# Performance work log

Hardware: AMD Instinct MI355X
Metric: run time of the kernel (lower is better)

The kernel has to match this reference:

```python
import jax, jax.numpy as jnp
import numpy as np

N_NODES = 50000
N_EDGES = 800000
IN_DIM = 128
HID = 256
HEADS = 4
OUT_DIM = 128
NEG_SLOPE = 0.2


def gat_conv(x, src, dst, W, a_src, a_dst, b, heads, out_ch):
    """PyG-style GATConv: per-edge attention + segment softmax over dst."""
    N = x.shape[0]
    h = (x @ W).reshape(N, heads, out_ch)              # [N,H,C]
    alph_s = jnp.einsum('nhc,hc->nh', h, a_src)        # [N,H]
    alph_d = jnp.einsum('nhc,hc->nh', h, a_dst)        # [N,H]
    e = jax.nn.leaky_relu(alph_s[src] + alph_d[dst], NEG_SLOPE)  # [E,H]
    m = jax.lax.stop_gradient(jax.ops.segment_max(e, dst, num_segments=N))
    ex = jnp.exp(e - m[dst])
    s = jax.ops.segment_sum(ex, dst, num_segments=N)
    alpha = ex / (s[dst] + 1e-16)                      # [E,H]
    out = jax.ops.segment_sum(h[src] * alpha[:, :, None], dst, num_segments=N)
    return out.reshape(N, heads * out_ch) + b


def setup_inputs() -> dict:
    key = jax.random.key(0)
    ks = jax.random.split(key, 12)
    x = jax.random.normal(ks[0], (N_NODES, IN_DIM), dtype=jnp.float32)
    edge_index = jax.random.randint(ks[1], (2, N_EDGES), 0, N_NODES, dtype=jnp.int64)
    c1 = HID // HEADS  # 64
    sc1 = 1.0 / np.sqrt(IN_DIM)
    sc2 = 1.0 / np.sqrt(HID)
    W1 = jax.random.normal(ks[2], (IN_DIM, HID), dtype=jnp.float32) * sc1
    a1_src = jax.random.normal(ks[3], (HEADS, c1), dtype=jnp.float32) * sc1
    a1_dst = jax.random.normal(ks[4], (HEADS, c1), dtype=jnp.float32) * sc1
    b1 = jnp.zeros((HID,), dtype=jnp.float32)
    W2 = jax.random.normal(ks[5], (HID, OUT_DIM), dtype=jnp.float32) * sc2
    a2_src = jax.random.normal(ks[6], (1, OUT_DIM), dtype=jnp.float32) * sc2
    a2_dst = jax.random.normal(ks[7], (1, OUT_DIM), dtype=jnp.float32) * sc2
    b2 = jnp.zeros((OUT_DIM,), dtype=jnp.float32)
    return {"x": x, "edge_index": edge_index, "W1": W1, "a1_src": a1_src,
            "a1_dst": a1_dst, "b1": b1, "W2": W2, "a2_src": a2_src,
            "a2_dst": a2_dst, "b2": b2}


def reference(x, edge_index, W1, a1_src, a1_dst, b1, W2, a2_src, a2_dst, b2):
    N = x.shape[0]
    loops = jnp.arange(N, dtype=edge_index.dtype)
    # PyG default add_self_loops=True
    src = jnp.concatenate([edge_index[0], loops])
    dst = jnp.concatenate([edge_index[1], loops])
    h = jax.nn.relu(gat_conv(x, src, dst, W1, a1_src, a1_dst, b1, HEADS, HID // HEADS))
    # dropout is identity in eval mode
    return gat_conv(h, src, dst, W2, a2_src, a2_dst, b2, 1, OUT_DIM)
```

## Files before the change

kernel.cpp:

```cpp
#include <hip/hip_runtime.h>
#include <math.h>

#define NEG_SLOPE 0.2f
#define SLOTS 64

typedef __attribute__((ext_vector_type(8))) short bf16x8;
typedef __attribute__((ext_vector_type(4))) float f32x4;
typedef __attribute__((ext_vector_type(2))) float f32x2;

__device__ __forceinline__ float lrelu(float t) {
    return t > 0.f ? t : NEG_SLOPE * t;
}
__device__ __forceinline__ unsigned short f2bf(float f) {
    unsigned u = __float_as_uint(f);
    unsigned r = (u + 0x7fff + ((u >> 16) & 1)) >> 16;
    return (unsigned short)r;
}
__device__ __forceinline__ f32x2 unpack2(unsigned v) {
    f32x2 r;
    r.x = __uint_as_float(v << 16);
    r.y = __uint_as_float(v & 0xffff0000u);
    return r;
}

__global__ void prep(const float* __restrict__ x, unsigned* __restrict__ x_bf2,
                     const float* __restrict__ W1, unsigned short* __restrict__ W1t,
                     const float* __restrict__ W2, unsigned short* __restrict__ W2t,
                     const float* __restrict__ a1s, const float* __restrict__ a1d,
                     float* __restrict__ vsd1,
                     const float* __restrict__ a2s, const float* __restrict__ a2d,
                     float* __restrict__ vsd2,
                     int* __restrict__ cursor, int* __restrict__ eSrc,
                     long nx2, int N, int n0, int n1, int n2, int n3, int n4) {
    const int b = blockIdx.x, t = threadIdx.x;
    if (b < n0) {
        long i = (long)b * 256 + t;
        if (i < nx2) {
            float2 v = ((const float2*)x)[i];
            x_bf2[i] = (unsigned)f2bf(v.x) | ((unsigned)f2bf(v.y) << 16);
        }
    } else if (b < n1) {
        int i = (b - n0) * 256 + t;
        if (i < 256 * 128) {
            int n = i / 128, k = i % 128;
            W1t[i] = f2bf(W1[k * 256 + n]);
        }
    } else if (b < n2) {
        int i = (b - n1) * 256 + t;
        if (i < 128 * 256) {
            int n = i / 256, k = i % 256;
            W2t[i] = f2bf(W2[k * 128 + n]);
        }
    } else if (b < n3) {
        int i = (b - n2) * 256 + t;
        if (i < 512) {
            int k = i / 4, h = i % 4;
            float s = 0.f, d = 0.f;
            for (int c = 0; c < 64; c++) {
                float wv = W1[k * 256 + h * 64 + c];
                s += wv * a1s[h * 64 + c];
                d += wv * a1d[h * 64 + c];
            }
            vsd1[h * 128 + k] = s;
            vsd1[(4 + h) * 128 + k] = d;
        }
    } else if (b < n4) {
        int i = (b - n3) * 256 + t;
        if (i < 256) {
            float s = 0.f, d = 0.f;
            for (int c = 0; c < 128; c++) {
                float wv = W2[i * 128 + c];
                s += wv * a2s[c];
                d += wv * a2d[c];
            }
            vsd2[i] = s;
            vsd2[256 + i] = d;
        }
    } else {
        int i = (b - n4) * 256 + t;
        if (i < N) {
            cursor[i] = 1;
            eSrc[i << 6] = i;
        }
    }
}

__global__ void scatter_edges(const int* __restrict__ src, const int* __restrict__ dst,
                              int* __restrict__ cursor, int* __restrict__ eSrc, int E) {
    int e = blockIdx.x * blockDim.x + threadIdx.x;
    if (e < E) {
        int d = dst[e];
        int pos = atomicAdd(&cursor[d], 1);
        if (pos < SLOTS) eSrc[(d << 6) + pos] = src[e];
    }
}

template <int K, int H>
__global__ void gemv_attn(const float* __restrict__ X, const float* __restrict__ vsd,
                          float* __restrict__ as_, float* __restrict__ ad_, int M) {
    __shared__ float vs[2 * H * K];
    int t = threadIdx.x;
    for (int i = t; i < 2 * H * K; i += 256) vs[i] = vsd[i];
    __syncthreads();
    int wave = t >> 6, lane = t & 63;
    int n = blockIdx.x * 4 + wave;
    if (n >= M) return;
    float acc[2 * H];
#pragma unroll
    for (int j = 0; j < 2 * H; j++) acc[j] = 0.f;
#pragma unroll
    for (int i = 0; i < K / 64; i++) {
        float xv = X[(size_t)n * K + i * 64 + lane];
#pragma unroll
        for (int j = 0; j < 2 * H; j++) acc[j] += xv * vs[j * K + i * 64 + lane];
    }
#pragma unroll
    for (int off = 32; off > 0; off >>= 1) {
#pragma unroll
        for (int j = 0; j < 2 * H; j++) acc[j] += __shfl_down(acc[j], off, 64);
    }
    if (lane == 0) {
#pragma unroll
        for (int h = 0; h < H; h++) {
            as_[n * H + h] = acc[h];
            ad_[n * H + h] = acc[H + h];
        }
    }
}

template <int K, int N>
__global__ __launch_bounds__(256) void gemm_mfma(const unsigned short* __restrict__ A,
                                                 const unsigned short* __restrict__ Bt,
                                                 unsigned short* __restrict__ Cb, int M) {
    constexpr int LDT = 72;
    __shared__ __align__(16) short As[128 * LDT];
    __shared__ __align__(16) short Bs[64 * LDT];
    const int t = threadIdx.x;
    const int wave = t >> 6, lane = t & 63;
    const int row0 = blockIdx.x * 128;
    const int n0 = blockIdx.y * 64;

    f32x4 acc[2][4];
#pragma unroll
    for (int mt = 0; mt < 2; mt++)
#pragma unroll
        for (int nt = 0; nt < 4; nt++) acc[mt][nt] = (f32x4){0.f, 0.f, 0.f, 0.f};

    const int r = t >> 3, c8 = (t & 7) * 8;
    for (int kc = 0; kc < K; kc += 64) {
        const unsigned short* srcA = A + (size_t)row0 * K + kc;
#pragma unroll
        for (int p = 0; p < 4; p++) {
            int rr = r + p * 32;
            *(bf16x8*)&As[rr * LDT + c8] = *(const bf16x8*)&srcA[(size_t)rr * K + c8];
        }
        const unsigned short* srcB = Bt + (size_t)n0 * K + kc;
#pragma unroll
        for (int p = 0; p < 2; p++) {
            int rr = r + p * 32;
            *(bf16x8*)&Bs[rr * LDT + c8] = *(const bf16x8*)&srcB[(size_t)rr * K + c8];
        }
        __syncthreads();

        const int mbase = wave * 32 + (lane & 15);
        const int quad = lane >> 4;
#pragma unroll
        for (int ks = 0; ks < 2; ks++) {
            int ko = ks * 32 + quad * 8;
            bf16x8 a0 = *(const bf16x8*)&As[mbase * LDT + ko];
            bf16x8 a1 = *(const bf16x8*)&As[(mbase + 16) * LDT + ko];
#pragma unroll
            for (int nt = 0; nt < 4; nt++) {
                bf16x8 b = *(const bf16x8*)&Bs[((lane & 15) + nt * 16) * LDT + ko];
                acc[0][nt] = __builtin_amdgcn_mfma_f32_16x16x32_bf16(a0, b, acc[0][nt], 0, 0, 0);
                acc[1][nt] = __builtin_amdgcn_mfma_f32_16x16x32_bf16(a1, b, acc[1][nt], 0, 0, 0);
            }
        }
        __syncthreads();
    }

    const int colb = n0 + (lane & 15);
    const int rquad = (lane >> 4) * 4;
#pragma unroll
    for (int mt = 0; mt < 2; mt++) {
        int rb = row0 + wave * 32 + mt * 16 + rquad;
#pragma unroll
        for (int nt = 0; nt < 4; nt++) {
#pragma unroll
            for (int rr2 = 0; rr2 < 4; rr2++) {
                int row = rb + rr2;
                if (row < M) Cb[(size_t)row * N + colb + nt * 16] = f2bf(acc[mt][nt][rr2]);
            }
        }
    }
}

__global__ __launch_bounds__(256) void gemm1_head(
    const unsigned short* __restrict__ agg, const unsigned short* __restrict__ W1t,
    const float* __restrict__ b1, const float* __restrict__ vsd2,
    unsigned short* __restrict__ out1b, float* __restrict__ as2, float* __restrict__ ad2,
    int M, int Mpad) {
    constexpr int K = 128, LDT = 72;
    __shared__ __align__(16) short As[128 * LDT];
    __shared__ __align__(16) short Bs[64 * LDT];
    const int t = threadIdx.x;
    const int wave = t >> 6, lane = t & 63;
    const int row0 = blockIdx.x * 128;
    const int h = blockIdx.y;
    const unsigned short* A = agg + (size_t)h * Mpad * K;
    const unsigned short* Bt = W1t + (size_t)h * 64 * K;

    f32x4 acc[2][4];
#pragma unroll
    for (int mt = 0; mt < 2; mt++)
#pragma unroll
        for (int nt = 0; nt < 4; nt++) acc[mt][nt] = (f32x4){0.f, 0.f, 0.f, 0.f};

    const int r = t >> 3, c8 = (t & 7) * 8;
    for (int kc = 0; kc < K; kc += 64) {
        const unsigned short* srcA = A + (size_t)row0 * K + kc;
#pragma unroll
        for (int p = 0; p < 4; p++) {
            int rr = r + p * 32;
            *(bf16x8*)&As[rr * LDT + c8] = *(const bf16x8*)&srcA[(size_t)rr * K + c8];
        }
        const unsigned short* srcB = Bt + kc;
#pragma unroll
        for (int p = 0; p < 2; p++) {
            int rr = r + p * 32;
            *(bf16x8*)&Bs[rr * LDT + c8] = *(const bf16x8*)&srcB[(size_t)rr * K + c8];
        }
        __syncthreads();

        const int mbase = wave * 32 + (lane & 15);
        const int quad = lane >> 4;
#pragma unroll
        for (int ks = 0; ks < 2; ks++) {
            int ko = ks * 32 + quad * 8;
            bf16x8 a0 = *(const bf16x8*)&As[mbase * LDT + ko];
            bf16x8 a1 = *(const bf16x8*)&As[(mbase + 16) * LDT + ko];
#pragma unroll
            for (int nt = 0; nt < 4; nt++) {
                bf16x8 b = *(const bf16x8*)&Bs[((lane & 15) + nt * 16) * LDT + ko];
                acc[0][nt] = __builtin_amdgcn_mfma_f32_16x16x32_bf16(a0, b, acc[0][nt], 0, 0, 0);
                acc[1][nt] = __builtin_amdgcn_mfma_f32_16x16x32_bf16(a1, b, acc[1][nt], 0, 0, 0);
            }
        }
        __syncthreads();
    }

    const int col16 = lane & 15;
    const int grp = lane >> 4;
#pragma unroll
    for (int mt = 0; mt < 2; mt++) {
        int rb = row0 + wave * 32 + mt * 16 + grp * 4;
#pragma unroll
        for (int rr = 0; rr < 4; rr++) {
            int row = rb + rr;
            float ps = 0.f, pd = 0.f;
#pragma unroll
            for (int nt = 0; nt < 4; nt++) {
                int cg = h * 64 + col16 + nt * 16;
                float rres = acc[mt][nt][rr] + b1[cg];
                rres = fmaxf(rres, 0.f);
                if (row < M) out1b[(size_t)row * 256 + cg] = f2bf(rres);
                ps += rres * vsd2[cg];
                pd += rres * vsd2[256 + cg];
            }
#pragma unroll
            for (int mask = 1; mask < 16; mask <<= 1) {
                ps += __shfl_xor(ps, mask, 64);
                pd += __shfl_xor(pd, mask, 64);
            }
            if (col16 == 0 && row < M) {
                atomicAdd(&as2[row], ps);
                atomicAdd(&ad2[row], pd);
            }
        }
    }
}

__global__ __launch_bounds__(256) void fused_gather1(
    const int* __restrict__ cursor, const int* __restrict__ eSrc,
    const unsigned short* __restrict__ Xb,
    const float* __restrict__ as_, const float* __restrict__ ad_,
    unsigned short* __restrict__ agg, int N, int Mpad) {
    const int wv = threadIdx.x >> 6, lane = threadIdx.x & 63;
    const int half = lane >> 5, hl = lane & 31;
    const int d = blockIdx.x * 8 + wv * 2 + half;

    __shared__ float4 alS[4][2][64];
    __shared__ int offS[4][2][64];

    const bool vn = d < N;
    int deg = 0;
    if (vn) { deg = cursor[d]; if (deg > SLOTS) deg = SLOTS; }
    float4 adv = make_float4(0.f, 0.f, 0.f, 0.f);
    if (vn) adv = ((const float4*)ad_)[d];

    const int beg = d << 6;
    const int j0 = hl, j1 = hl + 32;
    const bool a0 = j0 < deg, a1 = j1 < deg;
    int s0 = vn ? d : 0, s1 = vn ? d : 0;
    if (a0) s0 = eSrc[beg + j0];
    if (a1) s1 = eSrc[beg + j1];
    float4 q0 = make_float4(0.f, 0.f, 0.f, 0.f), q1 = q0;
    if (a0) q0 = ((const float4*)as_)[s0];
    if (a1) q1 = ((const float4*)as_)[s1];

    float qa0[4] = {q0.x, q0.y, q0.z, q0.w};
    float qa1[4] = {q1.x, q1.y, q1.z, q1.w};
    float ad4[4] = {adv.x, adv.y, adv.z, adv.w};
    float e0[4], e1[4], m[4];
#pragma unroll
    for (int h = 0; h < 4; h++) {
        e0[h] = a0 ? lrelu(qa0[h] + ad4[h]) : -1e30f;
        e1[h] = a1 ? lrelu(qa1[h] + ad4[h]) : -1e30f;
        m[h] = fmaxf(e0[h], e1[h]);
    }
#pragma unroll
    for (int off = 1; off < 32; off <<= 1)
#pragma unroll
        for (int h = 0; h < 4; h++) m[h] = fmaxf(m[h], __shfl_xor(m[h], off, 64));
    float x0[4], x1[4], sum[4];
#pragma unroll
    for (int h = 0; h < 4; h++) {
        x0[h] = a0 ? __expf(e0[h] - m[h]) : 0.f;
        x1[h] = a1 ? __expf(e1[h] - m[h]) : 0.f;
        sum[h] = x0[h] + x1[h];
    }
#pragma unroll
    for (int off = 1; off < 32; off <<= 1)
#pragma unroll
        for (int h = 0; h < 4; h++) sum[h] += __shfl_xor(sum[h], off, 64);
    float ri[4];
#pragma unroll
    for (int h = 0; h < 4; h++) ri[h] = 1.f / (sum[h] + 1e-16f);

    alS[wv][half][j0] = make_float4(x0[0] * ri[0], x0[1] * ri[1], x0[2] * ri[2], x0[3] * ri[3]);
    alS[wv][half][j1] = make_float4(x1[0] * ri[0], x1[1] * ri[1], x1[2] * ri[2], x1[3] * ri[3]);
    offS[wv][half][j0] = s0 << 8;
    offS[wv][half][j1] = s1 << 8;

    int dmax = deg;
    { int o = __shfl_xor(dmax, 32, 64); dmax = dmax > o ? dmax : o; }

    const char* Xc = (const char*)Xb;
    const int myoff = hl * 8;
    f32x2 acc[4][2];
#pragma unroll
    for (int h = 0; h < 4; h++) { acc[h][0] = (f32x2){0.f, 0.f}; acc[h][1] = (f32x2){0.f, 0.f}; }

    int j = 0;
    for (; j + 3 < dmax; j += 4) {
        int o0 = offS[wv][half][j], o1 = offS[wv][half][j + 1];
        int o2 = offS[wv][half][j + 2], o3 = offS[wv][half][j + 3];
        uint2 v0 = *(const uint2*)(Xc + o0 + myoff);
        uint2 v1 = *(const uint2*)(Xc + o1 + myoff);
        uint2 v2 = *(const uint2*)(Xc + o2 + myoff);
        uint2 v3 = *(const uint2*)(Xc + o3 + myoff);
        float4 al0 = alS[wv][half][j];
        float4 al1 = alS[wv][half][j + 1];
        float4 al2 = alS[wv][half][j + 2];
        float4 al3 = alS[wv][half][j + 3];
        {
            f32x2 lo = unpack2(v0.x), hi = unpack2(v0.y);
            acc[0][0] += al0.x * lo; acc[0][1] += al0.x * hi;
            acc[1][0] += al0.y * lo; acc[1][1] += al0.y * hi;
            acc[2][0] += al0.z * lo; acc[2][1] += al0.z * hi;
            acc[3][0] += al0.w * lo; acc[3][1] += al0.w * hi;
        }
        {
            f32x2 lo = unpack2(v1.x), hi = unpack2(v1.y);
            acc[0][0] += al1.x * lo; acc[0][1] += al1.x * hi;
            acc[1][0] += al1.y * lo; acc[1][1] += al1.y * hi;
            acc[2][0] += al1.z * lo; acc[2][1] += al1.z * hi;
            acc[3][0] += al1.w * lo; acc[3][1] += al1.w * hi;
        }
        {
            f32x2 lo = unpack2(v2.x), hi = unpack2(v2.y);
            acc[0][0] += al2.x * lo; acc[0][1] += al2.x * hi;
            acc[1][0] += al2.y * lo; acc[1][1] += al2.y * hi;
            acc[2][0] += al2.z * lo; acc[2][1] += al2.z * hi;
            acc[3][0] += al2.w * lo; acc[3][1] += al2.w * hi;
        }
        {
            f32x2 lo = unpack2(v3.x), hi = unpack2(v3.y);
            acc[0][0] += al3.x * lo; acc[0][1] += al3.x * hi;
            acc[1][0] += al3.y * lo; acc[1][1] += al3.y * hi;
            acc[2][0] += al3.z * lo; acc[2][1] += al3.z * hi;
            acc[3][0] += al3.w * lo; acc[3][1] += al3.w * hi;
        }
    }
    for (; j < dmax; j++) {
        int o0 = offS[wv][half][j];
        uint2 v0 = *(const uint2*)(Xc + o0 + myoff);
        float4 al0 = alS[wv][half][j];
        f32x2 lo = unpack2(v0.x), hi = unpack2(v0.y);
        acc[0][0] += al0.x * lo; acc[0][1] += al0.x * hi;
        acc[1][0] += al0.y * lo; acc[1][1] += al0.y * hi;
        acc[2][0] += al0.z * lo; acc[2][1] += al0.z * hi;
        acc[3][0] += al0.w * lo; acc[3][1] += al0.w * hi;
    }

    if (vn) {
#pragma unroll
        for (int h = 0; h < 4; h++) {
            uint2 pack;
            pack.x = (unsigned)f2bf(acc[h][0].x) | ((unsigned)f2bf(acc[h][0].y) << 16);
            pack.y = (unsigned)f2bf(acc[h][1].x) | ((unsigned)f2bf(acc[h][1].y) << 16);
            ((uint2*)(agg + ((size_t)h * Mpad + d) * 128))[hl] = pack;
        }
    }
}

__global__ __launch_bounds__(256) void fused_gather2(
    const int* __restrict__ cursor, const int* __restrict__ eSrc,
    const unsigned short* __restrict__ Hb,
    const float* __restrict__ as_, const float* __restrict__ ad_,
    const float* __restrict__ b2, float* __restrict__ out, int N) {
    const int wv = threadIdx.x >> 6, lane = threadIdx.x & 63;
    const int half = lane >> 5, hl = lane & 31;
    const int d = blockIdx.x * 8 + wv * 2 + half;

    __shared__ float alS[4][2][64];
    __shared__ int offS[4][2][64];

    const bool vn = d < N;
    int deg = 0;
    if (vn) { deg = cursor[d]; if (deg > SLOTS) deg = SLOTS; }
    const float adv = vn ? ad_[d] : 0.f;

    const int beg = d << 6;
    const int j0 = hl, j1 = hl + 32;
    const bool a0 = j0 < deg, a1 = j1 < deg;
    int s0 = vn ? d : 0, s1 = vn ? d : 0;
    if (a0) s0 = eSrc[beg + j0];
    if (a1) s1 = eSrc[beg + j1];
    float e0 = a0 ? lrelu(as_[s0] + adv) : -1e30f;
    float e1 = a1 ? lrelu(as_[s1] + adv) : -1e30f;
    float m = fmaxf(e0, e1);
#pragma unroll
    for (int off = 1; off < 32; off <<= 1) m = fmaxf(m, __shfl_xor(m, off, 64));
    float x0 = a0 ? __expf(e0 - m) : 0.f;
    float x1 = a1 ? __expf(e1 - m) : 0.f;
    float sum = x0 + x1;
#pragma unroll
    for (int off = 1; off < 32; off <<= 1) sum += __shfl_xor(sum, off, 64);
    float ri = 1.f / (sum + 1e-16f);

    alS[wv][half][j0] = x0 * ri;
    alS[wv][half][j1] = x1 * ri;
    offS[wv][half][j0] = s0 << 8;
    offS[wv][half][j1] = s1 << 8;

    int dmax = deg;
    { int o = __shfl_xor(dmax, 32, 64); dmax = dmax > o ? dmax : o; }

    const char* Hc = (const char*)Hb;
    const int myoff = hl * 8;
    f32x2 acc0 = (f32x2){0.f, 0.f}, acc1 = (f32x2){0.f, 0.f};

    int j = 0;
    for (; j + 3 < dmax; j += 4) {
        int o0 = offS[wv][half][j], o1 = offS[wv][half][j + 1];
        int o2 = offS[wv][half][j + 2], o3 = offS[wv][half][j + 3];
        uint2 v0 = *(const uint2*)(Hc + o0 + myoff);
        uint2 v1 = *(const uint2*)(Hc + o1 + myoff);
        uint2 v2 = *(const uint2*)(Hc + o2 + myoff);
        uint2 v3 = *(const uint2*)(Hc + o3 + myoff);
        float b0 = alS[wv][half][j], b1v = alS[wv][half][j + 1];
        float b2v = alS[wv][half][j + 2], b3 = alS[wv][half][j + 3];
        acc0 += b0 * unpack2(v0.x); acc1 += b0 * unpack2(v0.y);
        acc0 += b1v * unpack2(v1.x); acc1 += b1v * unpack2(v1.y);
        acc0 += b2v * unpack2(v2.x); acc1 += b2v * unpack2(v2.y);
        acc0 += b3 * unpack2(v3.x); acc1 += b3 * unpack2(v3.y);
    }
    for (; j < dmax; j++) {
        int o0 = offS[wv][half][j];
        uint2 v0 = *(const uint2*)(Hc + o0 + myoff);
        float b0 = alS[wv][half][j];
        acc0 += b0 * unpack2(v0.x); acc1 += b0 * unpack2(v0.y);
    }

    if (vn) {
        float4 bb = ((const float4*)b2)[hl];
        float4 o;
        o.x = acc0.x + bb.x;
        o.y = acc0.y + bb.y;
        o.z = acc1.x + bb.z;
        o.w = acc1.y + bb.w;
        ((float4*)(out + (size_t)d * 128))[hl] = o;
    }
}

extern "C" void kernel_launch(void* const* d_in, const int* in_sizes, int n_in,
                              void* d_out, int out_size, void* d_ws, size_t ws_size,
                              hipStream_t stream) {
    const float* x   = (const float*)d_in[0];
    const int*   ei  = (const int*)d_in[1];
    const float* W1  = (const float*)d_in[2];
    const float* a1s = (const float*)d_in[3];
    const float* a1d = (const float*)d_in[4];
    const float* b1  = (const float*)d_in[5];
    const float* W2  = (const float*)d_in[6];
    const float* a2s = (const float*)d_in[7];
    const float* a2d = (const float*)d_in[8];
    const float* b2  = (const float*)d_in[9];

    const int N = in_sizes[0] / 128;
    const int E = in_sizes[1] / 2;
    const int* srcIdx = ei;
    const int* dstIdx = ei + E;
    float* out = (float*)d_out;

    const int MT = (N + 127) / 128;
    const int M_pad = MT * 128;

    char* w = (char*)d_ws;
    unsigned short* x_bf  = (unsigned short*)w; w += (size_t)N * 128 * 2;
    unsigned short* agg   = (unsigned short*)w; w += (size_t)4 * M_pad * 128 * 2;
    unsigned short* out1b = (unsigned short*)w; w += (size_t)M_pad * 256 * 2;
    unsigned short* h2b   = (unsigned short*)w; w += (size_t)N * 128 * 2;
    unsigned short* W1t   = (unsigned short*)w; w += (size_t)128 * 256 * 2;
    unsigned short* W2t   = (unsigned short*)w; w += (size_t)256 * 128 * 2;
    float* vsd1 = (float*)w; w += (size_t)128 * 8 * 4;
    float* vsd2 = (float*)w; w += (size_t)256 * 2 * 4;
    float* as1  = (float*)w; w += (size_t)N * 4 * 4;
    float* ad1  = (float*)w; w += (size_t)N * 4 * 4;
    float* as2  = (float*)w; w += (size_t)N * 4;
    float* ad2  = (float*)w; w += (size_t)N * 4;
    int* cursor = (int*)w;  w += (size_t)N * 4;
    int* eSrc   = (int*)w;  w += (size_t)N * SLOTS * 4;

    hipMemsetAsync(as2, 0, (size_t)N * 4, stream);
    hipMemsetAsync(ad2, 0, (size_t)N * 4, stream);

    {
        long nx2 = (long)N * 64;
        int c0 = (int)((nx2 + 255) / 256);
        int n0 = c0;
        int n1 = n0 + 128;
        int n2 = n1 + 128;
        int n3 = n2 + 2;
        int n4 = n3 + 1;
        int total = n4 + (N + 255) / 256;
        prep<<<total, 256, 0, stream>>>(x, (unsigned*)x_bf, W1, W1t, W2, W2t,
                                        a1s, a1d, vsd1, a2s, a2d, vsd2,
                                        cursor, eSrc, nx2, N, n0, n1, n2, n3, n4);
    }

    scatter_edges<<<(E + 255) / 256, 256, 0, stream>>>(srcIdx, dstIdx, cursor, eSrc, E);

    gemv_attn<128, 4><<<(N + 3) / 4, 256, 0, stream>>>(x, vsd1, as1, ad1, N);
    fused_gather1<<<(N + 7) / 8, 256, 0, stream>>>(cursor, eSrc, x_bf, as1, ad1, agg, N, M_pad);
    gemm1_head<<<dim3(MT, 4), 256, 0, stream>>>(agg, W1t, b1, vsd2, out1b, as2, ad2, N, M_pad);

    gemm_mfma<256, 128><<<dim3(MT, 2), 256, 0, stream>>>(out1b, W2t, h2b, N);
    fused_gather2<<<(N + 7) / 8, 256, 0, stream>>>(cursor, eSrc, h2b, as2, ad2, b2, out, N);
}
```

Measured before the change: 284.2 us.

## Fuse edge scatter, casts and attention GEMV into one kernel with 16-bit indices

Merges the input prep, the edge bucketing scatter and the layer-1 attention GEMV into a single multi-role kernel. A tiny separate kernel now computes the attention projection vectors that the GEMV needs. Edge source ids are stored as 16-bit values, and each thread scatters four edges using vectorized loads. The self-loop is now implied as an extra row per node instead of being written into the bucket. The aim is to cut kernel launches and halve index memory traffic. In exchange, the 16-bit storage only works for fewer than 65536 nodes, and one bucket slot is lost to the cap of 63.

Result: slower. 294.1 us (+3.5%).

```diff
diff --git a/kernel.cpp b/kernel.cpp
--- a/kernel.cpp
+++ b/kernel.cpp
@@ -3,6 +3,7 @@
 
 #define NEG_SLOPE 0.2f
 #define SLOTS 64
+#define ECAP 63
 
 typedef __attribute__((ext_vector_type(8))) short bf16x8;
 typedef __attribute__((ext_vector_type(4))) float f32x4;
@@ -23,107 +24,110 @@
     return r;
 }
 
-__global__ void prep(const float* __restrict__ x, unsigned* __restrict__ x_bf2,
+__global__ void prep0(const float* __restrict__ W1, const float* __restrict__ a1s,
+                      const float* __restrict__ a1d, float* __restrict__ vsd1,
+                      const float* __restrict__ W2, const float* __restrict__ a2s,
+                      const float* __restrict__ a2d, float* __restrict__ vsd2) {
+    int i = blockIdx.x * 256 + threadIdx.x;
+    if (i < 512) {
+        int k = i >> 2, h = i & 3;
+        float s = 0.f, d = 0.f;
+        for (int c = 0; c < 64; c++) {
+            float wv = W1[k * 256 + h * 64 + c];
+            s += wv * a1s[h * 64 + c];
+            d += wv * a1d[h * 64 + c];
+        }
+        vsd1[h * 128 + k] = s;
+        vsd1[(4 + h) * 128 + k] = d;
+    } else if (i < 768) {
+        int j = i - 512;
+        float s = 0.f, d = 0.f;
+        for (int c = 0; c < 128; c++) {
+            float wv = W2[j * 128 + c];
+            s += wv * a2s[c];
+            d += wv * a2d[c];
+        }
+        vsd2[j] = s;
+        vsd2[256 + j] = d;
+    }
+}
+
+__global__ void mega(const int* __restrict__ src, const int* __restrict__ dst,
+                     int* __restrict__ cursor, unsigned short* __restrict__ eSrc,
+                     const float* __restrict__ x, uint4* __restrict__ xb4,
                      const float* __restrict__ W1, unsigned short* __restrict__ W1t,
                      const float* __restrict__ W2, unsigned short* __restrict__ W2t,
-                     const float* __restrict__ a1s, const float* __restrict__ a1d,
-                     float* __restrict__ vsd1,
-                     const float* __restrict__ a2s, const float* __restrict__ a2d,
-                     float* __restrict__ vsd2,
-                     int* __restrict__ cursor, int* __restrict__ eSrc,
-                     long nx2, int N, int n0, int n1, int n2, int n3, int n4) {
+                     const float* __restrict__ vsd1,
+                     float* __restrict__ as1, float* __restrict__ ad1,
+                     int E, int N, int bS, int bC, int bW1, int bW2) {
+    __shared__ float vs[1024];
     const int b = blockIdx.x, t = threadIdx.x;
-    if (b < n0) {
-        long i = (long)b * 256 + t;
-        if (i < nx2) {
-            float2 v = ((const float2*)x)[i];
-            x_bf2[i] = (unsigned)f2bf(v.x) | ((unsigned)f2bf(v.y) << 16);
-        }
-    } else if (b < n1) {
-        int i = (b - n0) * 256 + t;
-        if (i < 256 * 128) {
-            int n = i / 128, k = i % 128;
-            W1t[i] = f2bf(W1[k * 256 + n]);
-        }
-    } else if (b < n2) {
-        int i = (b - n1) * 256 + t;
-        if (i < 128 * 256) {
-            int n = i / 256, k = i % 256;
-            W2t[i] = f2bf(W2[k * 128 + n]);
-        }
-    } else if (b < n3) {
-        int i = (b - n2) * 256 + t;
-        if (i < 512) {
-            int k = i / 4, h = i % 4;
-            float s = 0.f, d = 0.f;
-            for (int c = 0; c < 64; c++) {
-                float wv = W1[k * 256 + h * 64 + c];
-                s += wv * a1s[h * 64 + c];
-                d += wv * a1d[h * 64 + c];
-            }
-            vsd1[h * 128 + k] = s;
-            vsd1[(4 + h) * 128 + k] = d;
-        }
-    } else if (b < n4) {
-        int i = (b - n3) * 256 + t;
-        if (i < 256) {
-            float s = 0.f, d = 0.f;
-            for (int c = 0; c < 128; c++) {
-                float wv = W2[i * 128 + c];
-                s += wv * a2s[c];
-                d += wv * a2d[c];
-            }
-            vsd2[i] = s;
-            vsd2[256 + i] = d;
-        }
+    if (b < bS) {
+        int i4 = (b * 256 + t) * 4;
+        if (i4 + 3 < E) {
+            const int4 s4 = *(const int4*)(src + i4);
+            const int4 d4 = *(const int4*)(dst + i4);
+            int p0 = atomicAdd(&cursor[d4.x], 1);
+            int p1 = atomicAdd(&cursor[d4.y], 1);
+            int p2 = atomicAdd(&cursor[d4.z], 1);
+            int p3 = atomicAdd(&cursor[d4.w], 1);
+            if (p0 < ECAP) eSrc[(d4.x << 6) + p0] = (unsigned short)s4.x;
+            if (p1 < ECAP) eSrc[(d4.y << 6) + p1] = (unsigned short)s4.y;
+            if (p2 < ECAP) eSrc[(d4.z << 6) + p2] = (unsigned short)s4.z;
+            if (p3 < ECAP) eSrc[(d4.w << 6) + p3] = (unsigned short)s4.w;
+        } else {
+            for (int k = i4; k < E && k < i4 + 4; k++) {
+                int d = dst[k];
+                int pos = atomicAdd(&cursor[d], 1);
+                if (pos < ECAP) eSrc[(d << 6) + pos] = (unsigned short)src[k];
+            }
+        }
+    } else if (b < bC) {
+        int i = (b - bS) * 256 + t;
+        if (i < N * 16) {
+            const float4* x4 = (const float4*)x;
+            float4 v0 = x4[2 * i], v1 = x4[2 * i + 1];
+            uint4 o;
+            o.x = (unsigned)f2bf(v0.x) | ((unsigned)f2bf(v0.y) << 16);
+            o.y = (unsigned)f2bf(v0.z) | ((unsigned)f2bf(v0.w) << 16);
+            o.z = (unsigned)f2bf(v1.x) | ((unsigned)f2bf(v1.y) << 16);
+            o.w = (unsigned)f2bf(v1.z) | ((unsigned)f2bf(v1.w) << 16);
+            xb4[i] = o;
+        }
+    } else if (b < bW1) {
+        int i = (b - bC) * 256 + t;
+        int n = i >> 7, k = i & 127;
+        W1t[i] = f2bf(W1[k * 256 + n]);
+    } else if (b < bW2) {
+        int i = (b - bW1) * 256 + t;
+        int n = i >> 8, k = i & 255;
+        W2t[i] = f2bf(W2[k * 128 + n]);
     } else {
-        int i = (b - n4) * 256 + t;
-        if (i < N) {
-            cursor[i] = 1;
-            eSrc[i << 6] = i;
-        }
-    }
-}
-
-__global__ void scatter_edges(const int* __restrict__ src, const int* __restrict__ dst,
-                              int* __restrict__ cursor, int* __restrict__ eSrc, int E) {
-    int e = blockIdx.x * blockDim.x + threadIdx.x;
-    if (e < E) {
-        int d = dst[e];
-        int pos = atomicAdd(&cursor[d], 1);
-        if (pos < SLOTS) eSrc[(d << 6) + pos] = src[e];
-    }
-}
-
-template <int K, int H>
-__global__ void gemv_attn(const float* __restrict__ X, const float* __restrict__ vsd,
-                          float* __restrict__ as_, float* __restrict__ ad_, int M) {
-    __shared__ float vs[2 * H * K];
-    int t = threadIdx.x;
-    for (int i = t; i < 2 * H * K; i += 256) vs[i] = vsd[i];
-    __syncthreads();
-    int wave = t >> 6, lane = t & 63;
-    int n = blockIdx.x * 4 + wave;
-    if (n >= M) return;
-    float acc[2 * H];
-#pragma unroll
-    for (int j = 0; j < 2 * H; j++) acc[j] = 0.f;
-#pragma unroll
-    for (int i = 0; i < K / 64; i++) {
-        float xv = X[(size_t)n * K + i * 64 + lane];
-#pragma unroll
-        for (int j = 0; j < 2 * H; j++) acc[j] += xv * vs[j * K + i * 64 + lane];
-    }
-#pragma unroll
-    for (int off = 32; off > 0; off >>= 1) {
-#pragma unroll
-        for (int j = 0; j < 2 * H; j++) acc[j] += __shfl_down(acc[j], off, 64);
-    }
-    if (lane == 0) {
-#pragma unroll
-        for (int h = 0; h < H; h++) {
-            as_[n * H + h] = acc[h];
-            ad_[n * H + h] = acc[H + h];
+        for (int i = t; i < 1024; i += 256) vs[i] = vsd1[i];
+        __syncthreads();
+        int wave = t >> 6, lane = t & 63;
+        int n = (b - bW2) * 4 + wave;
+        if (n >= N) return;
+        float acc[8];
+#pragma unroll
+        for (int j = 0; j < 8; j++) acc[j] = 0.f;
+#pragma unroll
+        for (int i = 0; i < 2; i++) {
+            float xv = x[(size_t)n * 128 + i * 64 + lane];
+#pragma unroll
+            for (int j = 0; j < 8; j++) acc[j] += xv * vs[j * 128 + i * 64 + lane];
+        }
+#pragma unroll
+        for (int off = 32; off > 0; off >>= 1) {
+#pragma unroll
+            for (int j = 0; j < 8; j++) acc[j] += __shfl_down(acc[j], off, 64);
+        }
+        if (lane == 0) {
+#pragma unroll
+            for (int h = 0; h < 4; h++) {
+                as1[n * 4 + h] = acc[h];
+                ad1[n * 4 + h] = acc[4 + h];
+            }
         }
     }
 }
@@ -281,7 +285,7 @@
 }
 
 __global__ __launch_bounds__(256) void fused_gather1(
-    const int* __restrict__ cursor, const int* __restrict__ eSrc,
+    const int* __restrict__ cursor, const unsigned short* __restrict__ eSrc,
     const unsigned short* __restrict__ Xb,
     const float* __restrict__ as_, const float* __restrict__ ad_,
     unsigned short* __restrict__ agg, int N, int Mpad) {
@@ -294,16 +298,16 @@
 
     const bool vn = d < N;
     int deg = 0;
-    if (vn) { deg = cursor[d]; if (deg > SLOTS) deg = SLOTS; }
+    if (vn) { deg = cursor[d]; if (deg > ECAP) deg = ECAP; }
     float4 adv = make_float4(0.f, 0.f, 0.f, 0.f);
     if (vn) adv = ((const float4*)ad_)[d];
 
     const int beg = d << 6;
     const int j0 = hl, j1 = hl + 32;
-    const bool a0 = j0 < deg, a1 = j1 < deg;
+    const bool a0 = vn && (j0 <= deg), a1 = vn && (j1 <= deg);
     int s0 = vn ? d : 0, s1 = vn ? d : 0;
-    if (a0) s0 = eSrc[beg + j0];
-    if (a1) s1 = eSrc[beg + j1];
+    if (vn && j0 < deg) s0 = eSrc[beg + j0];
+    if (vn && j1 < deg) s1 = eSrc[beg + j1];
     float4 q0 = make_float4(0.f, 0.f, 0.f, 0.f), q1 = q0;
     if (a0) q0 = ((const float4*)as_)[s0];
     if (a1) q1 = ((const float4*)as_)[s1];
@@ -342,8 +346,8 @@
     offS[wv][half][j0] = s0 << 8;
     offS[wv][half][j1] = s1 << 8;
 
-    int dmax = deg;
-    { int o = __shfl_xor(dmax, 32, 64); dmax = dmax > o ? dmax : o; }
+    int rows = vn ? deg + 1 : 0;
+    { int o = __shfl_xor(rows, 32, 64); rows = rows > o ? rows : o; }
 
     const char* Xc = (const char*)Xb;
     const int myoff = hl * 8;
@@ -352,7 +356,7 @@
     for (int h = 0; h < 4; h++) { acc[h][0] = (f32x2){0.f, 0.f}; acc[h][1] = (f32x2){0.f, 0.f}; }
 
     int j = 0;
-    for (; j + 3 < dmax; j += 4) {
+    for (; j + 3 < rows; j += 4) {
         int o0 = offS[wv][half][j], o1 = offS[wv][half][j + 1];
         int o2 = offS[wv][half][j + 2], o3 = offS[wv][half][j + 3];
         uint2 v0 = *(const uint2*)(Xc + o0 + myoff);
@@ -392,7 +396,7 @@
             acc[3][0] += al3.w * lo; acc[3][1] += al3.w * hi;
         }
     }
-    for (; j < dmax; j++) {
+    for (; j < rows; j++) {
         int o0 = offS[wv][half][j];
         uint2 v0 = *(const uint2*)(Xc + o0 + myoff);
         float4 al0 = alS[wv][half][j];
@@ -415,7 +419,7 @@
 }
 
 __global__ __launch_bounds__(256) void fused_gather2(
-    const int* __restrict__ cursor, const int* __restrict__ eSrc,
+    const int* __restrict__ cursor, const unsigned short* __restrict__ eSrc,
     const unsigned short* __restrict__ Hb,
     const float* __restrict__ as_, const float* __restrict__ ad_,
     const float* __restrict__ b2, float* __restrict__ out, int N) {
@@ -428,15 +432,15 @@
 
     const bool vn = d < N;
     int deg = 0;
-    if (vn) { deg = cursor[d]; if (deg > SLOTS) deg = SLOTS; }
+    if (vn) { deg = cursor[d]; if (deg > ECAP) deg = ECAP; }
     const float adv = vn ? ad_[d] : 0.f;
 
     const int beg = d << 6;
     const int j0 = hl, j1 = hl + 32;
-    const bool a0 = j0 < deg, a1 = j1 < deg;
+    const bool a0 = vn && (j0 <= deg), a1 = vn && (j1 <= deg);
     int s0 = vn ? d : 0, s1 = vn ? d : 0;
-    if (a0) s0 = eSrc[beg + j0];
-    if (a1) s1 = eSrc[beg + j1];
+    if (vn && j0 < deg) s0 = eSrc[beg + j0];
+    if (vn && j1 < deg) s1 = eSrc[beg + j1];
     float e0 = a0 ? lrelu(as_[s0] + adv) : -1e30f;
     float e1 = a1 ? lrelu(as_[s1] + adv) : -1e30f;
     float m = fmaxf(e0, e1);
@@ -454,15 +458,15 @@
     offS[wv][half][j0] = s0 << 8;
     offS[wv][half][j1] = s1 << 8;
 
-    int dmax = deg;
-    { int o = __shfl_xor(dmax, 32, 64); dmax = dmax > o ? dmax : o; }
+    int rows = vn ? deg + 1 : 0;
+    { int o = __shfl_xor(rows, 32, 64); rows = rows > o ? rows : o; }
 
     const char* Hc = (const char*)Hb;
     const int myoff = hl * 8;
     f32x2 acc0 = (f32x2){0.f, 0.f}, acc1 = (f32x2){0.f, 0.f};
 
     int j = 0;
-    for (; j + 3 < dmax; j += 4) {
+    for (; j + 3 < rows; j += 4) {
         int o0 = offS[wv][half][j], o1 = offS[wv][half][j + 1];
         int o2 = offS[wv][half][j + 2], o3 = offS[wv][half][j + 3];
         uint2 v0 = *(const uint2*)(Hc + o0 + myoff);
@@ -476,7 +480,7 @@
         acc0 += b2v * unpack2(v2.x); acc1 += b2v * unpack2(v2.y);
         acc0 += b3 * unpack2(v3.x); acc1 += b3 * unpack2(v3.y);
     }
-    for (; j < dmax; j++) {
+    for (; j < rows; j++) {
         int o0 = offS[wv][half][j];
         uint2 v0 = *(const uint2*)(Hc + o0 + myoff);
         float b0 = alS[wv][half][j];
@@ -531,28 +535,26 @@
     float* as2  = (float*)w; w += (size_t)N * 4;
     float* ad2  = (float*)w; w += (size_t)N * 4;
     int* cursor = (int*)w;  w += (size_t)N * 4;
-    int* eSrc   = (int*)w;  w += (size_t)N * SLOTS * 4;
-
+    unsigned short* eSrc = (unsigned short*)w; w += (size_t)N * SLOTS * 2;
+
+    hipMemsetAsync(cursor, 0, (size_t)N * 4, stream);
     hipMemsetAsync(as2, 0, (size_t)N * 4, stream);
     hipMemsetAsync(ad2, 0, (size_t)N * 4, stream);
 
+    prep0<<<3, 256, 0, stream>>>(W1, a1s, a1d, vsd1, W2, a2s, a2d, vsd2);
+
     {
-        long nx2 = (long)N * 64;
-        int c0 = (int)((nx2 + 255) / 256);
-        int n0 = c0;
-        int n1 = n0 + 128;
-        int n2 = n1 + 128;
-        int n3 = n2 + 2;
-        int n4 = n3 + 1;
-        int total = n4 + (N + 255) / 256;
-        prep<<<total, 256, 0, stream>>>(x, (unsigned*)x_bf, W1, W1t, W2, W2t,
-                                        a1s, a1d, vsd1, a2s, a2d, vsd2,
-                                        cursor, eSrc, nx2, N, n0, n1, n2, n3, n4);
-    }
-
-    scatter_edges<<<(E + 255) / 256, 256, 0, stream>>>(srcIdx, dstIdx, cursor, eSrc, E);
-
-    gemv_attn<128, 4><<<(N + 3) / 4, 256, 0, stream>>>(x, vsd1, as1, ad1, N);
+        const int bS  = (E + 1023) / 1024;
+        const int nC  = (N * 16 + 255) / 256;
+        const int bC  = bS + nC;
+        const int bW1 = bC + 128;
+        const int bW2 = bW1 + 128;
+        const int nG  = (N + 3) / 4;
+        mega<<<bW2 + nG, 256, 0, stream>>>(srcIdx, dstIdx, cursor, eSrc,
+                                           x, (uint4*)x_bf, W1, W1t, W2, W2t,
+                                           vsd1, as1, ad1, E, N, bS, bC, bW1, bW2);
+    }
+
     fused_gather1<<<(N + 7) / 8, 256, 0, stream>>>(cursor, eSrc, x_bf, as1, ad1, agg, N, M_pad);
     gemm1_head<<<dim3(MT, 4), 256, 0, stream>>>(agg, W1t, b1, vsd2, out1b, as2, ad2, N, M_pad);
 
```
